# Kernel optimization log

Hardware: AMD Instinct MI355X
Metric: run time of the kernel (lower is better)

Reference implementation:

```python
import jax, jax.numpy as jnp
import numpy as np

POS_W = 1.0
ANG_W = 1.0
WID_W = 1.0
N = 1048560  # predictions (divisible by 17)
M = 8388480  # total GT grasps = sum(arange(N) % 17)


def setup_inputs() -> dict:
    key = jax.random.key(0)
    k1, k2 = jax.random.split(key)
    pred = jax.random.normal(k1, (N, 6), dtype=jnp.float32)
    all_targets = jax.random.normal(k2, (M, 6), dtype=jnp.float32)
    # ragged counts in [0, 16]; sum == M exactly
    target_counts = (jnp.arange(N, dtype=jnp.int64) % 17)
    return {"pred": pred, "all_targets": all_targets, "target_counts": target_counts}


def _smooth_l1(x):
    a = jnp.abs(x)
    return jnp.where(a < 1.0, 0.5 * x * x, a - 0.5)


def reference(pred, all_targets, target_counts):
    n = pred.shape[0]
    m = all_targets.shape[0]
    # segment id for each GT row (contiguous slices, order of target_counts)
    seg = jnp.repeat(jnp.arange(n), target_counts, total_repeat_length=m)  # (M,)
    p = pred[seg]  # (M,6) gathered predictions
    dp = p[:, :2] - all_targets[:, :2]
    da = p[:, 2:4] - all_targets[:, 2:4]
    dw = p[:, 4] - all_targets[:, 4]
    dist = (POS_W * jnp.sum(dp * dp, axis=-1)
            + ANG_W * jnp.sum(da * da, axis=-1)
            + WID_W * dw * dw)  # (M,)
    # ragged argmin per segment (first occurrence, like torch.argmin)
    min_d = jax.ops.segment_min(dist, seg, num_segments=n)  # (N,)
    row = jnp.arange(m)
    cand = jnp.where(dist == min_d[seg], row, m)
    arg = jax.ops.segment_min(cand, seg, num_segments=n)  # (N,) global row idx or m
    has = target_counts > 0
    gt = all_targets[jnp.where(has, jnp.clip(arg, 0, m - 1), 0)]  # (N,6)
    # fused per-prediction loss against the closest GT
    loss_pos = jnp.sum(_smooth_l1(pred[:, :2] - gt[:, :2]), axis=-1)
    loss_ang = jnp.sum(jnp.abs(pred[:, 2:4] - gt[:, 2:4]), axis=-1)
    loss_wid = _smooth_l1(pred[:, 4] - gt[:, 4])
    losses = jnp.where(has, POS_W * loss_pos + ANG_W * loss_ang + WID_W * loss_wid, 0.0)
    return jnp.mean(losses)  # reduction='mean'
```

## Files before the change

### kernel.cpp

```cpp
#include <hip/hip_runtime.h>
#include <math.h>

#define POS_W 1.0f
#define ANG_W 1.0f
#define WID_W 1.0f
#define CHUNK 1024
#define F2PT 12

__device__ __forceinline__ float smooth_l1(float x) {
    float a = fabsf(x);
    return a < 1.0f ? 0.5f * x * x : a - 0.5f;
}

__global__ void k_block_sums(const int* __restrict__ counts, int stride, int n,
                             int* __restrict__ blockSums) {
    int i = blockIdx.x * 256 + threadIdx.x;
    int c = (i < n) ? counts[(long long)i * stride] : 0;
    for (int off = 32; off > 0; off >>= 1) c += __shfl_down(c, off, 64);
    __shared__ int sdata[4];
    int lane = threadIdx.x & 63, wave = threadIdx.x >> 6;
    if (lane == 0) sdata[wave] = c;
    __syncthreads();
    if (threadIdx.x == 0)
        blockSums[blockIdx.x] = sdata[0] + sdata[1] + sdata[2] + sdata[3];
}

__global__ void k_scan_blocks(const int* __restrict__ blockSums, int nb,
                              int* __restrict__ blockOffs) {
    int t = threadIdx.x;
    int per = (nb + 255) / 256;
    int start = t * per;
    int end = min(start + per, nb);
    int sum = 0;
    for (int j = start; j < end; ++j) sum += blockSums[j];
    __shared__ int s[256];
    s[t] = sum;
    __syncthreads();
    for (int d = 1; d < 256; d <<= 1) {
        int v = (t >= d) ? s[t - d] : 0;
        __syncthreads();
        s[t] += v;
        __syncthreads();
    }
    int run = s[t] - sum;
    for (int j = start; j < end; ++j) {
        blockOffs[j] = run;
        run += blockSums[j];
    }
}

__global__ __launch_bounds__(256) void k_loss(
    const float* __restrict__ pred, const float* __restrict__ tgt,
    const int* __restrict__ counts, int stride, int n,
    const int* __restrict__ blockOffs, float invN, float* __restrict__ out) {
    __shared__ float2 ch[CHUNK * 3];
    __shared__ int wsum[4];
    __shared__ float fs[4];

    int t = threadIdx.x;
    int lane = t & 63, wave = t >> 6;
    int i = blockIdx.x * 256 + t;
    int c = (i < n) ? counts[(long long)i * stride] : 0;

    int incl = c;
#pragma unroll
    for (int d = 1; d < 64; d <<= 1) {
        int v = __shfl_up(incl, d, 64);
        if (lane >= d) incl += v;
    }
    if (lane == 63) wsum[wave] = incl;
    __syncthreads();
    int w0 = wsum[0], w1 = wsum[1], w2 = wsum[2], w3 = wsum[3];
    int waveOff = (wave > 0 ? w0 : 0) + (wave > 1 ? w1 : 0) + (wave > 2 ? w2 : 0);
    int off = waveOff + incl - c;
    int total = w0 + w1 + w2 + w3;
    int winStart = blockOffs[blockIdx.x];

    bool active = (i < n) && (c > 0);
    float p0 = 0, p1 = 0, p2 = 0, p3 = 0, p4 = 0;
    if (active) {
        const float2* p2p = (const float2*)(pred + (long long)i * 6);
        float2 a = p2p[0], b = p2p[1], w = p2p[2];
        p0 = a.x; p1 = a.y; p2 = b.x; p3 = b.y; p4 = w.x;
    }

    float best = INFINITY;
    float b0 = 0, b1 = 0, b2 = 0, b3 = 0, b4 = 0;

    const float2* win = (const float2*)tgt + (long long)winStart * 3;
    float2 r[F2PT];

    {
        int nF2 = min(CHUNK, total) * 3;
#pragma unroll
        for (int j = 0; j < F2PT; ++j) {
            int k = t + 256 * j;
            if (k < nF2) r[j] = win[k];
        }
    }

    for (int base = 0; base < total; base += CHUNK) {
        int rows = min(CHUNK, total - base);
        int nF2c = rows * 3;
#pragma unroll
        for (int j = 0; j < F2PT; ++j) {
            int k = t + 256 * j;
            if (k < nF2c) ch[k] = r[j];
        }
        __syncthreads();
        int nbase = base + CHUNK;
        if (nbase < total) {
            int nF2n = min(CHUNK, total - nbase) * 3;
            const float2* srcn = win + (long long)nbase * 3;
#pragma unroll
            for (int j = 0; j < F2PT; ++j) {
                int k = t + 256 * j;
                if (k < nF2n) r[j] = srcn[k];
            }
        }
        if (active) {
            int lo = max(off, base), hi = min(off + c, base + rows);
            for (int rr = lo; rr < hi; ++rr) {
                int l3 = (rr - base) * 3;
                float2 ga = ch[l3], gb = ch[l3 + 1], gw = ch[l3 + 2];
                float d0 = p0 - ga.x, d1 = p1 - ga.y;
                float d2 = p2 - gb.x, d3 = p3 - gb.y;
                float d4 = p4 - gw.x;
                float dist = POS_W * (d0 * d0 + d1 * d1) +
                             ANG_W * (d2 * d2 + d3 * d3) + WID_W * d4 * d4;
                if (dist < best) {
                    best = dist;
                    b0 = ga.x; b1 = ga.y; b2 = gb.x; b3 = gb.y; b4 = gw.x;
                }
            }
        }
        __syncthreads();
    }

    float loss = 0.0f;
    if (active) {
        loss = POS_W * (smooth_l1(p0 - b0) + smooth_l1(p1 - b1)) +
               ANG_W * (fabsf(p2 - b2) + fabsf(p3 - b3)) +
               WID_W * smooth_l1(p4 - b4);
    }

    for (int o = 32; o > 0; o >>= 1) loss += __shfl_down(loss, o, 64);
    if (lane == 0) fs[wave] = loss;
    __syncthreads();
    if (t == 0) {
        float tot = (fs[0] + fs[1] + fs[2] + fs[3]) * invN;
        atomicAdd(out, tot);
    }
}

extern "C" void kernel_launch(void* const* d_in, const int* in_sizes, int n_in,
                              void* d_out, int out_size, void* d_ws,
                              size_t ws_size, hipStream_t stream) {
    const float* pred = (const float*)d_in[0];
    const float* tgt = (const float*)d_in[1];
    const int* counts = (const int*)d_in[2];
    int n = in_sizes[0] / 6;
    int stride = (in_sizes[2] == n) ? 1 : 2;
    int nb = (n + 255) / 256;

    int* blockSums = (int*)d_ws;
    int* blockOffs = blockSums + nb;
    float* out = (float*)d_out;

    hipMemsetAsync(d_out, 0, sizeof(float), stream);
    k_block_sums<<<nb, 256, 0, stream>>>(counts, stride, n, blockSums);
    k_scan_blocks<<<1, 256, 0, stream>>>(blockSums, nb, blockOffs);
    k_loss<<<nb, 256, 0, stream>>>(pred, tgt, counts, stride, n, blockOffs,
                                   1.0f / n, out);
}
```

Measured before the change: 309.6 us.

## Fold block-offset scan into loss kernel via redundant per-block prefix sums

Removes the single-block scan kernel and instead has each loss block sum all preceding block counts itself, with a wave reduction and shared-memory combine. This eliminates one serialized launch and its dependency gap. The cost is quadratic redundant reads of the block-sum array across blocks, which adds L2 traffic at the start of every block.

```diff
diff --git a/kernel.cpp b/kernel.cpp
--- a/kernel.cpp
+++ b/kernel.cpp
@@ -25,42 +25,23 @@
         blockSums[blockIdx.x] = sdata[0] + sdata[1] + sdata[2] + sdata[3];
 }
 
-__global__ void k_scan_blocks(const int* __restrict__ blockSums, int nb,
-                              int* __restrict__ blockOffs) {
-    int t = threadIdx.x;
-    int per = (nb + 255) / 256;
-    int start = t * per;
-    int end = min(start + per, nb);
-    int sum = 0;
-    for (int j = start; j < end; ++j) sum += blockSums[j];
-    __shared__ int s[256];
-    s[t] = sum;
-    __syncthreads();
-    for (int d = 1; d < 256; d <<= 1) {
-        int v = (t >= d) ? s[t - d] : 0;
-        __syncthreads();
-        s[t] += v;
-        __syncthreads();
-    }
-    int run = s[t] - sum;
-    for (int j = start; j < end; ++j) {
-        blockOffs[j] = run;
-        run += blockSums[j];
-    }
-}
-
 __global__ __launch_bounds__(256) void k_loss(
     const float* __restrict__ pred, const float* __restrict__ tgt,
     const int* __restrict__ counts, int stride, int n,
-    const int* __restrict__ blockOffs, float invN, float* __restrict__ out) {
+    const int* __restrict__ blockSums, float invN, float* __restrict__ out) {
     __shared__ float2 ch[CHUNK * 3];
     __shared__ int wsum[4];
+    __shared__ int wpre[4];
     __shared__ float fs[4];
 
     int t = threadIdx.x;
     int lane = t & 63, wave = t >> 6;
-    int i = blockIdx.x * 256 + t;
+    int b = blockIdx.x;
+    int i = b * 256 + t;
     int c = (i < n) ? counts[(long long)i * stride] : 0;
+
+    int pre = 0;
+    for (int j = t; j < b; j += 256) pre += blockSums[j];
 
     int incl = c;
 #pragma unroll
@@ -68,21 +49,24 @@
         int v = __shfl_up(incl, d, 64);
         if (lane >= d) incl += v;
     }
+    for (int o = 32; o > 0; o >>= 1) pre += __shfl_down(pre, o, 64);
     if (lane == 63) wsum[wave] = incl;
+    if (lane == 0) wpre[wave] = pre;
+
+    bool active = (i < n) && (c > 0);
+    float p0 = 0, p1 = 0, p2 = 0, p3 = 0, p4 = 0;
+    if (active) {
+        const float2* p2p = (const float2*)(pred + (long long)i * 6);
+        float2 a = p2p[0], bb = p2p[1], w = p2p[2];
+        p0 = a.x; p1 = a.y; p2 = bb.x; p3 = bb.y; p4 = w.x;
+    }
+
     __syncthreads();
     int w0 = wsum[0], w1 = wsum[1], w2 = wsum[2], w3 = wsum[3];
     int waveOff = (wave > 0 ? w0 : 0) + (wave > 1 ? w1 : 0) + (wave > 2 ? w2 : 0);
     int off = waveOff + incl - c;
     int total = w0 + w1 + w2 + w3;
-    int winStart = blockOffs[blockIdx.x];
-
-    bool active = (i < n) && (c > 0);
-    float p0 = 0, p1 = 0, p2 = 0, p3 = 0, p4 = 0;
-    if (active) {
-        const float2* p2p = (const float2*)(pred + (long long)i * 6);
-        float2 a = p2p[0], b = p2p[1], w = p2p[2];
-        p0 = a.x; p1 = a.y; p2 = b.x; p3 = b.y; p4 = w.x;
-    }
+    int winStart = wpre[0] + wpre[1] + wpre[2] + wpre[3];
 
     float best = INFINITY;
     float b0 = 0, b1 = 0, b2 = 0, b3 = 0, b4 = 0;
@@ -164,12 +148,10 @@
     int nb = (n + 255) / 256;
 
     int* blockSums = (int*)d_ws;
-    int* blockOffs = blockSums + nb;
     float* out = (float*)d_out;
 
     hipMemsetAsync(d_out, 0, sizeof(float), stream);
     k_block_sums<<<nb, 256, 0, stream>>>(counts, stride, n, blockSums);
-    k_scan_blocks<<<1, 256, 0, stream>>>(blockSums, nb, blockOffs);
-    k_loss<<<nb, 256, 0, stream>>>(pred, tgt, counts, stride, n, blockOffs,
+    k_loss<<<nb, 256, 0, stream>>>(pred, tgt, counts, stride, n, blockSums,
                                    1.0f / n, out);
 }
```

Measured after the change: 308.0 us. About the same (-0.5%).
